# Kernel tuning notes

Measured on AMD Instinct MI355X. Metric: run time of the kernel, lower is better.

Reference implementation:

```python
import jax, jax.numpy as jnp
import numpy as np

C = 64  # RDN out_dim

def _make_coord_1d(n):
    r = 1.0 / n
    return -1.0 + r + 2.0 * r * jnp.arange(n, dtype=jnp.float32)

def _unfold3x3(feat):
    # torch F.unfold(feat, 3, padding=1) -> [B, C*9, H, W], ordering c*9 + (ki*3+kj)
    B, Cc, H, W = feat.shape
    p = jnp.pad(feat, ((0, 0), (0, 0), (1, 1), (1, 1)))
    patches = jnp.stack([p[:, :, di:di + H, dj:dj + W]
                         for di in range(3) for dj in range(3)], axis=2)
    return patches.reshape(B, Cc * 9, H, W)

def setup_inputs() -> dict:
    key = jax.random.key(0)
    ks = jax.random.split(key, 5)
    feat = jax.random.normal(ks[0], (1, C, 64, 64), dtype=jnp.float32)
    w1 = jax.random.normal(ks[1], (3, 256), dtype=jnp.float32) * 0.1
    b1 = jax.random.normal(ks[2], (256,), dtype=jnp.float32) * 0.01
    w2 = jax.random.normal(ks[3], (256, C * 9 * 3), dtype=jnp.float32) * 0.02
    b2 = jax.random.normal(ks[4], (C * 9 * 3,), dtype=jnp.float32) * 0.01
    return {"feat": feat, "w1": w1, "b1": b1, "w2": w2, "b2": b2,
            "out_h": 256, "out_w": 256}

def reference(feat, w1, b1, w2, b2, out_h, out_w):
    B, Cc, H, W = feat.shape
    C9 = Cc * 9
    # HR query coords at grid centers, flattened: [q, 2] (dim0 -> H axis)
    cy = _make_coord_1d(out_h)
    cx = _make_coord_1d(out_w)
    coord = jnp.stack(jnp.meshgrid(cy, cx, indexing='ij'), axis=-1).reshape(-1, 2)
    coord = jnp.broadcast_to(coord[None], (B, out_h * out_w, 2))  # [B, q, 2]
    cell = jnp.stack([jnp.full((out_h * out_w,), 2.0 / out_h, jnp.float32),
                      jnp.full((out_h * out_w,), 2.0 / out_w, jnp.float32)], axis=-1)
    cell = jnp.broadcast_to(cell[None], (B, out_h * out_w, 2))

    featu = _unfold3x3(feat)  # [B, C*9, H, W]

    # coord_ = coord - cell/2, clamped query coords
    coord_ = coord - cell * 0.5
    eps = 1e-6
    coord_q = jnp.clip(coord_ + eps, -1.0 + eps, 1.0 - eps)

    # grid_sample nearest, align_corners=False: idx = round(((c+1)*N - 1)/2)
    iy = jnp.clip(jnp.round(((coord_q[..., 0] + 1.0) * H - 1.0) * 0.5), 0, H - 1).astype(jnp.int32)
    ix = jnp.clip(jnp.round(((coord_q[..., 1] + 1.0) * W - 1.0) * 0.5), 0, W - 1).astype(jnp.int32)

    # gather unfolded features at nearest LR cells -> [B, q, C*9]
    q_feat = jax.vmap(lambda f, y, x: f[:, y, x])(featu, iy, ix)  # [B, C9, q]
    q_feat = jnp.swapaxes(q_feat, 1, 2)

    # feat_coord (shifted by half a cell) at gathered indices = -1 + 2*i/N
    q_coord0 = -1.0 + 2.0 * iy.astype(jnp.float32) / H
    q_coord1 = -1.0 + 2.0 * ix.astype(jnp.float32) / W

    rel0 = (coord_[..., 0] - q_coord0) * (H * 0.5)
    rel1 = (coord_[..., 1] - q_coord1) * (W * 0.5)
    r_rev = cell[..., 0] * (H * 0.5)
    mlp_in = jnp.stack([rel0, rel1, r_rev], axis=-1)  # [B, q, 3]

    h = jax.nn.relu(jnp.einsum('bqi,ih->bqh', mlp_in, w1) + b1)
    pred_w = (jnp.einsum('bqh,ho->bqo', h, w2) + b2).reshape(B, -1, C9, 3)

    # per-query 1xC9 @ C9x3 bmm
    rgb = jnp.einsum('bqc,bqco->bqo', q_feat, pred_w)  # [B, q, 3]
    return rgb.reshape(B, out_h, out_w, 3).transpose(0, 3, 1, 2)
```

## Files before the change

### kernel.cpp

```cpp
#include <hip/hip_runtime.h>


#define NOUT 1728

typedef short bf16x8 __attribute__((ext_vector_type(8)));
typedef float f32x4  __attribute__((ext_vector_type(4)));

__device__ inline unsigned bf16pack(float a, float b) {
    unsigned ua = __builtin_bit_cast(unsigned, a);
    unsigned ub = __builtin_bit_cast(unsigned, b);
    ua = (ua + 0x7FFFu + ((ua >> 16) & 1u)) >> 16;
    ub = (ub + 0x7FFFu + ((ub >> 16) & 1u)) >> 16;
    return ua | (ub << 16);
}

__global__ __launch_bounds__(256) void k_predw(
    const float* __restrict__ w1, const float* __restrict__ b1,
    const float* __restrict__ w2, const float* __restrict__ b2,
    unsigned short* __restrict__ predw16)
{
    __shared__ float h[256];
    __shared__ float red[256];
    const int tid   = threadIdx.x;
    const int s     = blockIdx.x / 27;
    const int chunk = blockIdx.x - s * 27;

    const float rel0 = (float)(s >> 2) * 0.25f;
    const float rel1 = (float)(s & 3) * 0.25f;

    float pre = fmaf(w1[tid], rel0,
                fmaf(w1[256 + tid], rel1,
                fmaf(w1[512 + tid], 0.25f, b1[tid])));
    h[tid] = fmaxf(pre, 0.0f);
    __syncthreads();

    const int olocal = tid & 63;
    const int q      = tid >> 6;
    const int o      = chunk * 64 + olocal;
    const float* w2c = w2 + q * 64 * NOUT + o;
    const float* hq  = h + q * 64;

    float acc = 0.0f;
    #pragma unroll 8
    for (int j = 0; j < 64; ++j)
        acc = fmaf(hq[j], w2c[j * NOUT], acc);
    red[tid] = acc;
    __syncthreads();

    if (tid < 64) {
        const int oo = chunk * 64 + tid;
        float a = red[tid] + red[tid + 64] + red[tid + 128] + red[tid + 192]
                + b2[oo];
        const int ct = oo / 3;
        const int k  = oo - ct * 3;
        const int c  = (ct * 7282) >> 16;
        const int tp = ct - c * 9;
        const int m  = s * 3 + k;
        const unsigned ub =
            (__builtin_bit_cast(unsigned, a) + 0x7FFFu +
             ((__builtin_bit_cast(unsigned, a) >> 16) & 1u)) >> 16;
        predw16[m * 576 + tp * 64 + c] = (unsigned short)ub;
    }
}

__global__ __launch_bounds__(192) void k_conv(
    const float* __restrict__ feat, const unsigned short* __restrict__ predw16,
    float* __restrict__ out)
{
    const int tid  = threadIdx.x;
    const int lane = tid & 63;
    const int mt   = tid >> 6;
    const int n    = blockIdx.x;
    const int y0   = n >> 2;
    const int x0   = (n & 3) << 4;

    const int lc = lane & 15;
    const int lk = lane >> 4;

    int xadr[3]; float xmsk[3];
    #pragma unroll
    for (int d = 0; d < 3; ++d) {
        const int rx = x0 + lc + d - 1;
        xmsk[d] = ((unsigned)rx < 64u) ? 1.0f : 0.0f;
        xadr[d] = rx < 0 ? 0 : (rx > 63 ? 63 : rx);
    }
    int yadr[3]; float ymsk[3];
    #pragma unroll
    for (int d = 0; d < 3; ++d) {
        const int ry = y0 + d - 1;
        ymsk[d] = ((unsigned)ry < 64u) ? 1.0f : 0.0f;
        yadr[d] = (ry < 0 ? 0 : (ry > 63 ? 63 : ry)) << 6;
    }

    const unsigned short* arow = predw16 + (mt * 16 + lc) * 576 + (lk << 3);

    f32x4 acc = {0.0f, 0.0f, 0.0f, 0.0f};

    #pragma unroll 2
    for (int kk = 0; kk < 18; ++kk) {
        const int tap = kk >> 1;
        const int dr  = (tap >= 6) ? 2 : (tap >= 3 ? 1 : 0);
        const int dc  = tap - dr * 3;
        const int c0  = ((kk & 1) << 5) + (lk << 3);
        const float* fb = feat + (c0 << 12) + yadr[dr] + xadr[dc];
        const float  mk = ymsk[dr] * xmsk[dc];

        float v0 = fb[0]         * mk;
        float v1 = fb[1 << 12]   * mk;
        float v2 = fb[2 << 12]   * mk;
        float v3 = fb[3 << 12]   * mk;
        float v4 = fb[4 << 12]   * mk;
        float v5 = fb[5 << 12]   * mk;
        float v6 = fb[6 << 12]   * mk;
        float v7 = fb[7 << 12]   * mk;

        uint4 bb;
        bb.x = bf16pack(v0, v1);
        bb.y = bf16pack(v2, v3);
        bb.z = bf16pack(v4, v5);
        bb.w = bf16pack(v6, v7);
        const bf16x8 bfrag = __builtin_bit_cast(bf16x8, bb);

        const bf16x8 afrag = *(const bf16x8*)(arow + 32 * kk);

        acc = __builtin_amdgcn_mfma_f32_16x16x32_bf16(afrag, bfrag, acc, 0, 0, 0);
    }

    #pragma unroll
    for (int r = 0; r < 4; ++r) {
        const int m = mt * 16 + (lk << 2) + r;
        const int s = (m * 171) >> 9;
        const int k = m - s * 3;
        const int y = (y0 << 2) + (s >> 2);
        const int x = ((x0 + lc) << 2) + (s & 3);
        out[k * 65536 + y * 256 + x] = acc[r];
    }
}

extern "C" void kernel_launch(void* const* d_in, const int* in_sizes, int n_in,
                              void* d_out, int out_size, void* d_ws, size_t ws_size,
                              hipStream_t stream) {
    const float* feat = (const float*)d_in[0];
    const float* w1   = (const float*)d_in[1];
    const float* b1   = (const float*)d_in[2];
    const float* w2   = (const float*)d_in[3];
    const float* b2   = (const float*)d_in[4];
    float* out = (float*)d_out;
    unsigned short* predw16 = (unsigned short*)d_ws;

    hipLaunchKernelGGL(k_predw, dim3(432), dim3(256), 0, stream,
                       w1, b1, w2, b2, predw16);
    hipLaunchKernelGGL(k_conv, dim3(256), dim3(192), 0, stream,
                       feat, predw16, out);
}
```

Baseline: 16.54 us.

## Fuse predw and conv kernels into one cooperative kernel with grid sync

Merges the weight-generation kernel and the MFMA conv kernel into a single cooperative launch of 256 blocks, separated by a grid-wide barrier. The predw stage is redistributed as 16 chunks of 108 outputs per sample, with a 2-way split over the hidden dimension instead of 4-way. This removes one kernel launch and the gap between launches, at the cost of cooperative launch overhead, a grid sync, and longer serial dot products of 128 per thread.

```diff
diff --git a/kernel.cpp b/kernel.cpp
--- a/kernel.cpp
+++ b/kernel.cpp
@@ -1,4 +1,7 @@
 #include <hip/hip_runtime.h>
+#include <hip/hip_cooperative_groups.h>
+
+namespace cg = cooperative_groups;
 
 
 #define NOUT 1728
@@ -6,6 +9,10 @@
 typedef short bf16x8 __attribute__((ext_vector_type(8)));
 typedef float f32x4  __attribute__((ext_vector_type(4)));
 
+__device__ inline unsigned short bf16r(float a) {
+    const unsigned ua = __builtin_bit_cast(unsigned, a);
+    return (unsigned short)((ua + 0x7FFFu + ((ua >> 16) & 1u)) >> 16);
+}
 __device__ inline unsigned bf16pack(float a, float b) {
     unsigned ua = __builtin_bit_cast(unsigned, a);
     unsigned ub = __builtin_bit_cast(unsigned, b);
@@ -14,126 +21,128 @@
     return ua | (ub << 16);
 }
 
-__global__ __launch_bounds__(256) void k_predw(
-    const float* __restrict__ w1, const float* __restrict__ b1,
-    const float* __restrict__ w2, const float* __restrict__ b2,
-    unsigned short* __restrict__ predw16)
+__global__ __launch_bounds__(256) void k_fused(
+    const float* __restrict__ feat, const float* __restrict__ w1,
+    const float* __restrict__ b1,   const float* __restrict__ w2,
+    const float* __restrict__ b2,   unsigned short* __restrict__ predw16,
+    float* __restrict__ out)
 {
     __shared__ float h[256];
-    __shared__ float red[256];
-    const int tid   = threadIdx.x;
-    const int s     = blockIdx.x / 27;
-    const int chunk = blockIdx.x - s * 27;
+    __shared__ float hred[216];
 
-    const float rel0 = (float)(s >> 2) * 0.25f;
-    const float rel1 = (float)(s & 3) * 0.25f;
+    const int tid = threadIdx.x;
+    const int bid = blockIdx.x;
 
-    float pre = fmaf(w1[tid], rel0,
-                fmaf(w1[256 + tid], rel1,
-                fmaf(w1[512 + tid], 0.25f, b1[tid])));
-    h[tid] = fmaxf(pre, 0.0f);
-    __syncthreads();
+    {
+        const int s     = bid >> 4;
+        const int chunk = bid & 15;
 
-    const int olocal = tid & 63;
-    const int q      = tid >> 6;
-    const int o      = chunk * 64 + olocal;
-    const float* w2c = w2 + q * 64 * NOUT + o;
-    const float* hq  = h + q * 64;
+        const float rel0 = (float)(s >> 2) * 0.25f;
+        const float rel1 = (float)(s & 3) * 0.25f;
 
-    float acc = 0.0f;
-    #pragma unroll 8
-    for (int j = 0; j < 64; ++j)
-        acc = fmaf(hq[j], w2c[j * NOUT], acc);
-    red[tid] = acc;
-    __syncthreads();
+        float pre = fmaf(w1[tid], rel0,
+                    fmaf(w1[256 + tid], rel1,
+                    fmaf(w1[512 + tid], 0.25f, b1[tid])));
+        h[tid] = fmaxf(pre, 0.0f);
+        __syncthreads();
 
-    if (tid < 64) {
-        const int oo = chunk * 64 + tid;
-        float a = red[tid] + red[tid + 64] + red[tid + 128] + red[tid + 192]
-                + b2[oo];
-        const int ct = oo / 3;
-        const int k  = oo - ct * 3;
-        const int c  = (ct * 7282) >> 16;
-        const int tp = ct - c * 9;
-        const int m  = s * 3 + k;
-        const unsigned ub =
-            (__builtin_bit_cast(unsigned, a) + 0x7FFFu +
-             ((__builtin_bit_cast(unsigned, a) >> 16) & 1u)) >> 16;
-        predw16[m * 576 + tp * 64 + c] = (unsigned short)ub;
-    }
-}
+        if (tid < 216) {
+            const int t  = tid >> 1;
+            const int kh = tid & 1;
+            const int o  = chunk * 108 + t;
+            const float* w2c = w2 + kh * 128 * NOUT + o;
+            const float* hq  = h + kh * 128;
+            float acc = 0.0f;
+            #pragma unroll 8
+            for (int j = 0; j < 128; ++j)
+                acc = fmaf(hq[j], w2c[j * NOUT], acc);
+            hred[tid] = acc;
+        }
+        __syncthreads();
 
-__global__ __launch_bounds__(192) void k_conv(
-    const float* __restrict__ feat, const unsigned short* __restrict__ predw16,
-    float* __restrict__ out)
-{
-    const int tid  = threadIdx.x;
-    const int lane = tid & 63;
-    const int mt   = tid >> 6;
-    const int n    = blockIdx.x;
-    const int y0   = n >> 2;
-    const int x0   = (n & 3) << 4;
-
-    const int lc = lane & 15;
-    const int lk = lane >> 4;
-
-    int xadr[3]; float xmsk[3];
-    #pragma unroll
-    for (int d = 0; d < 3; ++d) {
-        const int rx = x0 + lc + d - 1;
-        xmsk[d] = ((unsigned)rx < 64u) ? 1.0f : 0.0f;
-        xadr[d] = rx < 0 ? 0 : (rx > 63 ? 63 : rx);
-    }
-    int yadr[3]; float ymsk[3];
-    #pragma unroll
-    for (int d = 0; d < 3; ++d) {
-        const int ry = y0 + d - 1;
-        ymsk[d] = ((unsigned)ry < 64u) ? 1.0f : 0.0f;
-        yadr[d] = (ry < 0 ? 0 : (ry > 63 ? 63 : ry)) << 6;
+        if (tid < 108) {
+            const int o = chunk * 108 + tid;
+            const float a = hred[2 * tid] + hred[2 * tid + 1] + b2[o];
+            const int ct = o / 3;
+            const int k  = o - ct * 3;
+            const int c  = (ct * 7282) >> 16;
+            const int tp = ct - c * 9;
+            const int m  = s * 3 + k;
+            predw16[m * 576 + tp * 64 + c] = bf16r(a);
+        }
     }
 
-    const unsigned short* arow = predw16 + (mt * 16 + lc) * 576 + (lk << 3);
+    cg::this_grid().sync();
 
-    f32x4 acc = {0.0f, 0.0f, 0.0f, 0.0f};
+    if (tid < 192) {
+        const int lane = tid & 63;
+        const int mt   = tid >> 6;
+        const int n    = bid;
+        const int y0   = n >> 2;
+        const int x0   = (n & 3) << 4;
 
-    #pragma unroll 2
-    for (int kk = 0; kk < 18; ++kk) {
-        const int tap = kk >> 1;
-        const int dr  = (tap >= 6) ? 2 : (tap >= 3 ? 1 : 0);
-        const int dc  = tap - dr * 3;
-        const int c0  = ((kk & 1) << 5) + (lk << 3);
-        const float* fb = feat + (c0 << 12) + yadr[dr] + xadr[dc];
-        const float  mk = ymsk[dr] * xmsk[dc];
+        const int lc = lane & 15;
+        const int lk = lane >> 4;
 
-        float v0 = fb[0]         * mk;
-        float v1 = fb[1 << 12]   * mk;
-        float v2 = fb[2 << 12]   * mk;
-        float v3 = fb[3 << 12]   * mk;
-        float v4 = fb[4 << 12]   * mk;
-        float v5 = fb[5 << 12]   * mk;
-        float v6 = fb[6 << 12]   * mk;
-        float v7 = fb[7 << 12]   * mk;
+        int xadr[3]; float xmsk[3];
+        #pragma unroll
+        for (int d = 0; d < 3; ++d) {
+            const int rx = x0 + lc + d - 1;
+            xmsk[d] = ((unsigned)rx < 64u) ? 1.0f : 0.0f;
+            xadr[d] = rx < 0 ? 0 : (rx > 63 ? 63 : rx);
+        }
+        int yadr[3]; float ymsk[3];
+        #pragma unroll
+        for (int d = 0; d < 3; ++d) {
+            const int ry = y0 + d - 1;
+            ymsk[d] = ((unsigned)ry < 64u) ? 1.0f : 0.0f;
+            yadr[d] = (ry < 0 ? 0 : (ry > 63 ? 63 : ry)) << 6;
+        }
 
-        uint4 bb;
-        bb.x = bf16pack(v0, v1);
-        bb.y = bf16pack(v2, v3);
-        bb.z = bf16pack(v4, v5);
-        bb.w = bf16pack(v6, v7);
-        const bf16x8 bfrag = __builtin_bit_cast(bf16x8, bb);
+        const unsigned short* arow = predw16 + (mt * 16 + lc) * 576 + (lk << 3);
 
-        const bf16x8 afrag = *(const bf16x8*)(arow + 32 * kk);
+        f32x4 acc = {0.0f, 0.0f, 0.0f, 0.0f};
 
-        acc = __builtin_amdgcn_mfma_f32_16x16x32_bf16(afrag, bfrag, acc, 0, 0, 0);
-    }
+        #pragma unroll 2
+        for (int kk = 0; kk < 18; ++kk) {
+            const int tap = kk >> 1;
+            const int dr  = (tap >= 6) ? 2 : (tap >= 3 ? 1 : 0);
+            const int dc  = tap - dr * 3;
+            const int c0  = ((kk & 1) << 5) + (lk << 3);
+            const float* fb = feat + (c0 << 12) + yadr[dr] + xadr[dc];
+            const float  mk = ymsk[dr] * xmsk[dc];
 
-    #pragma unroll
-    for (int r = 0; r < 4; ++r) {
-        const int m = mt * 16 + (lk << 2) + r;
-        const int s = (m * 171) >> 9;
-        const int k = m - s * 3;
-        const int y = (y0 << 2) + (s >> 2);
-        const int x = ((x0 + lc) << 2) + (s & 3);
-        out[k * 65536 + y * 256 + x] = acc[r];
+            const float v0 = fb[0]       * mk;
+            const float v1 = fb[1 << 12] * mk;
+            const float v2 = fb[2 << 12] * mk;
+            const float v3 = fb[3 << 12] * mk;
+            const float v4 = fb[4 << 12] * mk;
+            const float v5 = fb[5 << 12] * mk;
+            const float v6 = fb[6 << 12] * mk;
+            const float v7 = fb[7 << 12] * mk;
+
+            uint4 bb;
+            bb.x = bf16pack(v0, v1);
+            bb.y = bf16pack(v2, v3);
+            bb.z = bf16pack(v4, v5);
+            bb.w = bf16pack(v6, v7);
+            const bf16x8 bfrag = __builtin_bit_cast(bf16x8, bb);
+
+            const bf16x8 afrag = *(const bf16x8*)(arow + 32 * kk);
+
+            acc = __builtin_amdgcn_mfma_f32_16x16x32_bf16(afrag, bfrag, acc,
+                                                          0, 0, 0);
+        }
+
+        #pragma unroll
+        for (int r = 0; r < 4; ++r) {
+            const int m = mt * 16 + (lk << 2) + r;
+            const int s = (m * 171) >> 9;
+            const int k = m - s * 3;
+            const int y = (y0 << 2) + (s >> 2);
+            const int x = ((x0 + lc) << 2) + (s & 3);
+            out[k * 65536 + y * 256 + x] = acc[r];
+        }
     }
 }
 
@@ -148,8 +157,8 @@
     float* out = (float*)d_out;
     unsigned short* predw16 = (unsigned short*)d_ws;
 
-    hipLaunchKernelGGL(k_predw, dim3(432), dim3(256), 0, stream,
-                       w1, b1, w2, b2, predw16);
-    hipLaunchKernelGGL(k_conv, dim3(256), dim3(192), 0, stream,
-                       feat, predw16, out);
+    void* args[] = {(void*)&feat, (void*)&w1, (void*)&b1, (void*)&w2,
+                    (void*)&b2, (void*)&predw16, (void*)&out};
+    hipLaunchCooperativeKernel(reinterpret_cast<void*>(k_fused),
+                               dim3(256), dim3(256), args, 0, stream);
 }
```

Measured after the change: 54.14 us. 3.27x slower.

## Split conv K-loop across four waves with LDS reduction and more blocks

Applied to the files above, without the earlier changes.

The conv kernel now launches one block per (M-tile, N-tile) pair, giving three times as many blocks. Inside each block, four waves each take a strided subset of the 18 K-steps, and their partial MFMA accumulators are summed through shared memory before wave 0 writes the output. This is meant to raise parallelism and hide latency on a small grid that underfilled the GPU. The cost is a barrier, LDS traffic, idle waves during the final store, and unbalanced work (5 vs 4 steps per wave). The predw inner loop unroll also goes from 8 to 16.

```diff
diff --git a/kernel.cpp b/kernel.cpp
--- a/kernel.cpp
+++ b/kernel.cpp
@@ -6,6 +6,10 @@
 typedef short bf16x8 __attribute__((ext_vector_type(8)));
 typedef float f32x4  __attribute__((ext_vector_type(4)));
 
+__device__ inline unsigned short bf16r(float a) {
+    const unsigned ua = __builtin_bit_cast(unsigned, a);
+    return (unsigned short)((ua + 0x7FFFu + ((ua >> 16) & 1u)) >> 16);
+}
 __device__ inline unsigned bf16pack(float a, float b) {
     unsigned ua = __builtin_bit_cast(unsigned, a);
     unsigned ub = __builtin_bit_cast(unsigned, b);
@@ -41,7 +45,7 @@
     const float* hq  = h + q * 64;
 
     float acc = 0.0f;
-    #pragma unroll 8
+    #pragma unroll 16
     for (int j = 0; j < 64; ++j)
         acc = fmaf(hq[j], w2c[j * NOUT], acc);
     red[tid] = acc;
@@ -56,23 +60,24 @@
         const int c  = (ct * 7282) >> 16;
         const int tp = ct - c * 9;
         const int m  = s * 3 + k;
-        const unsigned ub =
-            (__builtin_bit_cast(unsigned, a) + 0x7FFFu +
-             ((__builtin_bit_cast(unsigned, a) >> 16) & 1u)) >> 16;
-        predw16[m * 576 + tp * 64 + c] = (unsigned short)ub;
+        predw16[m * 576 + tp * 64 + c] = bf16r(a);
     }
 }
 
-__global__ __launch_bounds__(192) void k_conv(
+__global__ __launch_bounds__(256) void k_conv(
     const float* __restrict__ feat, const unsigned short* __restrict__ predw16,
     float* __restrict__ out)
 {
+    __shared__ f32x4 red[3 * 64];
+
     const int tid  = threadIdx.x;
     const int lane = tid & 63;
-    const int mt   = tid >> 6;
-    const int n    = blockIdx.x;
-    const int y0   = n >> 2;
-    const int x0   = (n & 3) << 4;
+    const int w    = tid >> 6;
+    const int bid  = blockIdx.x;
+    const int mt   = bid >> 8;
+    const int nt   = bid & 255;
+    const int y0   = nt >> 2;
+    const int x0   = (nt & 3) << 4;
 
     const int lc = lane & 15;
     const int lk = lane >> 4;
@@ -96,44 +101,57 @@
 
     f32x4 acc = {0.0f, 0.0f, 0.0f, 0.0f};
 
-    #pragma unroll 2
-    for (int kk = 0; kk < 18; ++kk) {
-        const int tap = kk >> 1;
-        const int dr  = (tap >= 6) ? 2 : (tap >= 3 ? 1 : 0);
-        const int dc  = tap - dr * 3;
-        const int c0  = ((kk & 1) << 5) + (lk << 3);
-        const float* fb = feat + (c0 << 12) + yadr[dr] + xadr[dc];
-        const float  mk = ymsk[dr] * xmsk[dc];
+    #pragma unroll
+    for (int i = 0; i < 5; ++i) {
+        const int kk = w + (i << 2);
+        if (kk < 18) {
+            const int tap = kk >> 1;
+            const int dr  = (tap >= 6) ? 2 : (tap >= 3 ? 1 : 0);
+            const int dc  = tap - dr * 3;
+            const int c0  = ((kk & 1) << 5) + (lk << 3);
+            const float* fb = feat + (c0 << 12) + yadr[dr] + xadr[dc];
+            const float  mk = ymsk[dr] * xmsk[dc];
 
-        float v0 = fb[0]         * mk;
-        float v1 = fb[1 << 12]   * mk;
-        float v2 = fb[2 << 12]   * mk;
-        float v3 = fb[3 << 12]   * mk;
-        float v4 = fb[4 << 12]   * mk;
-        float v5 = fb[5 << 12]   * mk;
-        float v6 = fb[6 << 12]   * mk;
-        float v7 = fb[7 << 12]   * mk;
+            const float v0 = fb[0]       * mk;
+            const float v1 = fb[1 << 12] * mk;
+            const float v2 = fb[2 << 12] * mk;
+            const float v3 = fb[3 << 12] * mk;
+            const float v4 = fb[4 << 12] * mk;
+            const float v5 = fb[5 << 12] * mk;
+            const float v6 = fb[6 << 12] * mk;
+            const float v7 = fb[7 << 12] * mk;
 
-        uint4 bb;
-        bb.x = bf16pack(v0, v1);
-        bb.y = bf16pack(v2, v3);
-        bb.z = bf16pack(v4, v5);
-        bb.w = bf16pack(v6, v7);
-        const bf16x8 bfrag = __builtin_bit_cast(bf16x8, bb);
+            uint4 bb;
+            bb.x = bf16pack(v0, v1);
+            bb.y = bf16pack(v2, v3);
+            bb.z = bf16pack(v4, v5);
+            bb.w = bf16pack(v6, v7);
+            const bf16x8 bfrag = __builtin_bit_cast(bf16x8, bb);
+            const bf16x8 afrag = *(const bf16x8*)(arow + 32 * kk);
 
-        const bf16x8 afrag = *(const bf16x8*)(arow + 32 * kk);
-
-        acc = __builtin_amdgcn_mfma_f32_16x16x32_bf16(afrag, bfrag, acc, 0, 0, 0);
+            acc = __builtin_amdgcn_mfma_f32_16x16x32_bf16(afrag, bfrag, acc,
+                                                          0, 0, 0);
+        }
     }
 
-    #pragma unroll
-    for (int r = 0; r < 4; ++r) {
-        const int m = mt * 16 + (lk << 2) + r;
-        const int s = (m * 171) >> 9;
-        const int k = m - s * 3;
-        const int y = (y0 << 2) + (s >> 2);
-        const int x = ((x0 + lc) << 2) + (s & 3);
-        out[k * 65536 + y * 256 + x] = acc[r];
+    if (w > 0) red[(w - 1) * 64 + lane] = acc;
+    __syncthreads();
+
+    if (w == 0) {
+        #pragma unroll
+        for (int q = 0; q < 3; ++q) {
+            const f32x4 v = red[q * 64 + lane];
+            acc[0] += v[0]; acc[1] += v[1]; acc[2] += v[2]; acc[3] += v[3];
+        }
+        #pragma unroll
+        for (int r = 0; r < 4; ++r) {
+            const int m = mt * 16 + (lk << 2) + r;
+            const int s = (m * 171) >> 9;
+            const int k = m - s * 3;
+            const int y = (y0 << 2) + (s >> 2);
+            const int x = ((x0 + lc) << 2) + (s & 3);
+            out[k * 65536 + y * 256 + x] = acc[r];
+        }
     }
 }
 
@@ -150,6 +168,6 @@
 
     hipLaunchKernelGGL(k_predw, dim3(432), dim3(256), 0, stream,
                        w1, b1, w2, b2, predw16);
-    hipLaunchKernelGGL(k_conv, dim3(256), dim3(192), 0, stream,
+    hipLaunchKernelGGL(k_conv, dim3(768), dim3(256), 0, stream,
                        feat, predw16, out);
 }
```

After: 14.26 us, median of 2. -13.7%, faster.
